# Kernel optimization log

Measured on AMD Instinct MI355X. Metric: run time of the kernel, lower is better.

## Reference

```python
import jax, jax.numpy as jnp
import numpy as np

B, L, D, H = 4, 2048, 1024, 16
DK = D // H  # 64


def setup_inputs() -> dict:
    key = jax.random.key(0)
    ks = jax.random.split(key, 5)
    x = jax.random.normal(ks[0], (B, L, D), dtype=jnp.float32)
    scale = 1.0 / np.sqrt(D)
    W_qkv = jax.random.normal(ks[1], (D, 3 * D), dtype=jnp.float32) * scale
    b_qkv = jnp.zeros((3 * D,), dtype=jnp.float32)
    W_out = jax.random.normal(ks[2], (D, D), dtype=jnp.float32) * scale
    b_out = jnp.zeros((D,), dtype=jnp.float32)
    return {"x": x, "W_qkv": W_qkv, "b_qkv": b_qkv, "W_out": W_out, "b_out": b_out}


def reference(x, W_qkv, b_qkv, W_out, b_out):
    Bx, Lx, Dx = x.shape
    qkv = x @ W_qkv + b_qkv                      # [B, L, 3D]
    q, k, v = jnp.split(qkv, 3, axis=-1)
    # [B, H, L, d_k]
    q = q.reshape(Bx, Lx, H, DK).transpose(0, 2, 1, 3)
    k = k.reshape(Bx, Lx, H, DK).transpose(0, 2, 1, 3)
    v = v.reshape(Bx, Lx, H, DK).transpose(0, 2, 1, 3)
    scores = jnp.einsum('bhqd,bhkd->bhqk', q, k) / np.sqrt(DK)
    causal = jnp.tril(jnp.ones((Lx, Lx), dtype=bool))
    scores = jnp.where(causal[None, None], scores, -jnp.inf)
    attn = jax.nn.softmax(scores, axis=-1)       # [B, H, L, L]
    out = jnp.einsum('bhqk,bhkd->bhqd', attn, v)
    out = out.transpose(0, 2, 1, 3).reshape(Bx, Lx, Dx)
    return out @ W_out + b_out
```

## Files before the change

kernel.cpp:

```cpp
#include <hip/hip_runtime.h>
#include <stdint.h>

#define B_ 4
#define L_ 2048
#define D_ 1024
#define H_ 16
#define DK_ 64

typedef __attribute__((ext_vector_type(8))) short bf16x8;
typedef __attribute__((ext_vector_type(4))) float f32x4;
typedef unsigned short bfu;

#define MFMA(a, b, c) __builtin_amdgcn_mfma_f32_16x16x32_bf16((a), (b), (c), 0, 0, 0)

__device__ __forceinline__ unsigned short f2bf(float f) {
  union { float f; unsigned int u; } v; v.f = f;
  unsigned int u = v.u;
  return (unsigned short)((u + 0x7fffu + ((u >> 16) & 1u)) >> 16);
}

__device__ __forceinline__ void gll16(const void* g, void* l) {
  __builtin_amdgcn_global_load_lds(
      (const __attribute__((address_space(1))) void*)g,
      (__attribute__((address_space(3))) void*)l, 16, 0, 0);
}

#define VMCNT(n_) asm volatile("s_waitcnt vmcnt(" #n_ ")" ::: "memory")
#define BARRIER() asm volatile("s_barrier" ::: "memory")

template <int N> __device__ __forceinline__ void vmwait() {
  static_assert(N >= 0 && N <= 8, "vmcnt range");
  if constexpr (N == 0) VMCNT(0);
  else if constexpr (N == 1) VMCNT(1);
  else if constexpr (N == 2) VMCNT(2);
  else if constexpr (N == 3) VMCNT(3);
  else if constexpr (N == 4) VMCNT(4);
  else if constexpr (N == 5) VMCNT(5);
  else if constexpr (N == 6) VMCNT(6);
  else if constexpr (N == 7) VMCNT(7);
  else VMCNT(8);
}


__global__ __launch_bounds__(256) void cast_x(const float* __restrict__ in,
                                              bfu* __restrict__ out, int n4) {
  int i = blockIdx.x * 256 + threadIdx.x;
  if (i >= n4) return;
  float4 v = ((const float4*)in)[i];
  ushort4 o;
  o.x = f2bf(v.x); o.y = f2bf(v.y); o.z = f2bf(v.z); o.w = f2bf(v.w);
  ((ushort4*)out)[i] = o;
}

__global__ void transpose_cast(const float* __restrict__ in, bfu* __restrict__ out,
                               int R, int C) {
  __shared__ float tile[32][33];
  int c0 = blockIdx.x * 32, r0 = blockIdx.y * 32;
  int tx = threadIdx.x, ty = threadIdx.y;
#pragma unroll
  for (int i = ty; i < 32; i += 8)
    tile[i][tx] = in[(size_t)(r0 + i) * C + c0 + tx];
  __syncthreads();
#pragma unroll
  for (int i = ty; i < 32; i += 8)
    out[(size_t)(c0 + i) * R + r0 + tx] = f2bf(tile[tx][i]);
}


template <int EPI, int BM, int BN, int WM, int WN>
__global__ __launch_bounds__(512, 4) void gemm8(
    const bfu* __restrict__ A, const bfu* __restrict__ Bt,
    const float* __restrict__ bias, bfu* __restrict__ Qg, bfu* __restrict__ Kg,
    bfu* __restrict__ Vtg, float* __restrict__ Out, int M, int N, int K) {
  __shared__ __align__(16) bfu LDSb[(BM + BN) * 128];
  constexpr int RM = BM / WM, RN = BN / WN;
  constexpr int MH = RM / 32, NH = RN / 32;
  constexpr int HA = BM / 128, HB = BN / 128;
  constexpr int LO = HA + HB;

  const int tid = threadIdx.x;
  const int lane = tid & 63;
  const int w = tid >> 6;
  const int wm = w / WN, wn = w % WN;
  const int l15 = lane & 15, l4 = lane >> 4;

  const int nwg = gridDim.x;
  const int cpx = nwg >> 3;
  const int bid = (int)blockIdx.x;
  const int swz = (bid & 7) * cpx + (bid >> 3);
  const int MT = M / BM;
  const int m0 = (swz % MT) * BM;
  const int n0 = (swz / MT) * BN;

  auto stageA = [&](int t, int half) {
    bfu* lb = LDSb + (t & 1) * (BM * 64);
#pragma unroll
    for (int j = 0; j < HA; ++j) {
      int idx = j * 512 + tid;
      int u = idx >> 3;
      int row = half * (RM / 2) + (u & (RM / 2 - 1)) + (u / (RM / 2)) * RM;
      int c16 = (idx & 7) ^ (row & 7);
      gll16(A + (size_t)(m0 + row) * K + t * 64 + c16 * 8,
            (char*)lb + row * 128 + (idx & 7) * 16);
    }
  };
  auto stageB = [&](int t, int half) {
    bfu* lb = LDSb + 2 * BM * 64 + (t & 1) * (BN * 64);
#pragma unroll
    for (int j = 0; j < HB; ++j) {
      int idx = j * 512 + tid;
      int u = idx >> 3;
      int row = half * (RN / 2) + (u & (RN / 2 - 1)) + (u / (RN / 2)) * RN;
      int c16 = (idx & 7) ^ (row & 7);
      gll16(Bt + (size_t)(n0 + row) * K + t * 64 + c16 * 8,
            (char*)lb + row * 128 + (idx & 7) * 16);
    }
  };

  f32x4 acc[2 * MH][2 * NH] = {};
  bf16x8 af[MH][2], bfLO[NH][2], bfHI[NH][2];

  auto lda = [&](int c, int half) {
    const char* base = (const char*)(LDSb + c * (BM * 64));
#pragma unroll
    for (int mi = 0; mi < MH; ++mi)
#pragma unroll
      for (int kk = 0; kk < 2; ++kk) {
        int row = wm * RM + half * (RM / 2) + mi * 16 + l15;
        int ch = (kk * 4 + l4) ^ (row & 7);
        af[mi][kk] = *(const bf16x8*)(base + row * 128 + ch * 16);
      }
  };
  auto ldb = [&](int c, int half, bf16x8 (&dst)[NH][2]) {
    const char* base = (const char*)(LDSb + 2 * BM * 64 + c * (BN * 64));
#pragma unroll
    for (int ni = 0; ni < NH; ++ni)
#pragma unroll
      for (int kk = 0; kk < 2; ++kk) {
        int row = wn * RN + half * (RN / 2) + ni * 16 + l15;
        int ch = (kk * 4 + l4) ^ (row & 7);
        dst[ni][kk] = *(const bf16x8*)(base + row * 128 + ch * 16);
      }
  };
  auto mm = [&](int mo, int no, bf16x8 (&bx)[NH][2]) {
    __builtin_amdgcn_s_setprio(1);
#pragma unroll
    for (int mi = 0; mi < MH; ++mi)
#pragma unroll
      for (int ni = 0; ni < NH; ++ni)
#pragma unroll
        for (int kk = 0; kk < 2; ++kk)
          acc[mo + mi][no + ni] = MFMA(af[mi][kk], bx[ni][kk], acc[mo + mi][no + ni]);
    __builtin_amdgcn_s_setprio(0);
  };

  stageA(0, 0); stageB(0, 0); stageB(0, 1); stageA(0, 1);
  vmwait<HB + HA>();
  BARRIER();

  const int NT = K >> 6;
  for (int t = 0; t < NT - 1; ++t) {
    const int c = t & 1, tn = t + 1;
    lda(c, 0); ldb(c, 0, bfLO);
    stageA(tn, 0); stageB(tn, 0);
    mm(0, 0, bfLO);
    vmwait<HA + LO>(); BARRIER();
    ldb(c, 1, bfHI);
    stageB(tn, 1);
    mm(0, NH, bfHI);
    vmwait<LO + HB>(); BARRIER();
    lda(c, 1);
    stageA(tn, 1);
    mm(MH, NH, bfHI);
    BARRIER();
    mm(MH, 0, bfLO);
    vmwait<HB + HA>(); BARRIER();
  }
  {
    const int c = (NT - 1) & 1;
    lda(c, 0); ldb(c, 0, bfLO);
    mm(0, 0, bfLO);
    vmwait<HA>(); BARRIER();
    ldb(c, 1, bfHI);
    mm(0, NH, bfHI);
    vmwait<0>(); BARRIER();
    lda(c, 1);
    mm(MH, NH, bfHI);
    mm(MH, 0, bfLO);
  }

  if constexpr (EPI == 1) {
#pragma unroll
    for (int ni = 0; ni < 2 * NH; ++ni) {
      int gn = n0 + wn * RN + ni * 16 + l15;
      float bv = bias[gn];
#pragma unroll
      for (int mi = 0; mi < 2 * MH; ++mi)
#pragma unroll
        for (int rg = 0; rg < 4; ++rg) {
          int gm = m0 + wm * RM + mi * 16 + l4 * 4 + rg;
          Out[(size_t)gm * N + gn] = acc[mi][ni][rg] + bv;
        }
    }
  } else {
    const int sec = n0 >> 10;
    if (sec < 2) {
      bfu* dst = (sec == 0) ? Qg : Kg;
      const float scale = (sec == 0) ? 0.18033688011112042f : 1.0f;
#pragma unroll
      for (int ni = 0; ni < 2 * NH; ++ni) {
        int gn = n0 + wn * RN + ni * 16 + l15;
        int rem = gn & 1023;
        int hh = rem >> 6, dk = rem & 63;
        float bv = bias[gn];
#pragma unroll
        for (int mi = 0; mi < 2 * MH; ++mi)
#pragma unroll
          for (int rg = 0; rg < 4; ++rg) {
            int gm = m0 + wm * RM + mi * 16 + l4 * 4 + rg;
            int bb = gm >> 11, ll = gm & 2047;
            dst[(((size_t)(bb * H_ + hh)) * L_ + ll) * DK_ + dk] =
                f2bf((acc[mi][ni][rg] + bv) * scale);
          }
      }
    } else {
      __syncthreads();
#pragma unroll
      for (int ni = 0; ni < 2 * NH; ++ni) {
        int n_local = wn * RN + ni * 16 + l15;
        int gn = n0 + n_local;
        float bv = bias[gn];
        int swzn = (n_local & 7) << 4;
#pragma unroll
        for (int mi = 0; mi < 2 * MH; ++mi) {
          int m_base = wm * RM + mi * 16 + l4 * 4;
          int k6 = m_base & 63;
          int p0 = (m_base & ~63) |
                   ((k6 & 32) | (((k6 >> 2) & 3) << 3) | (((k6 >> 4) & 1) << 2));
          float v0 = acc[mi][ni][0] + bv, v1 = acc[mi][ni][1] + bv;
          float v2 = acc[mi][ni][2] + bv, v3 = acc[mi][ni][3] + bv;
          uint32_t w01, w23;
          asm("v_cvt_pk_bf16_f32 %0, %1, %2" : "=v"(w01) : "v"(v0), "v"(v1));
          asm("v_cvt_pk_bf16_f32 %0, %1, %2" : "=v"(w23) : "v"(v2), "v"(v3));
          *(uint32_t*)((char*)LDSb + n_local * (BM * 2) + ((2 * p0) ^ swzn)) = w01;
          *(uint32_t*)((char*)LDSb + n_local * (BM * 2) + ((2 * p0 + 4) ^ swzn)) = w23;
        }
      }
      __syncthreads();
      int n = tid >> 2;
      int cb = (tid & 3) * 4;
      int gnn = n0 + n;
      int hh = (gnn >> 6) & 15, dk = gnn & 63;
      size_t rowbase =
          (((size_t)((m0 >> 11) * H_ + hh)) * DK_ + dk) * L_ + (m0 & 2047);
#pragma unroll
      for (int j = 0; j < 4; ++j) {
        int ch = cb + j;
        bf16x8 vv = *(const bf16x8*)((char*)LDSb + n * (BM * 2) +
                                     ((ch * 16) ^ ((n & 7) << 4)));
        *(bf16x8*)(Vtg + rowbase + ch * 8) = vv;
      }
    }
  }
}


__global__ __launch_bounds__(256, 3) void attn(const bfu* __restrict__ Qg,
                                               const bfu* __restrict__ Kg,
                                               const bfu* __restrict__ Vtg,
                                               bfu* __restrict__ Ao) {
  __shared__ __align__(16) bfu Ks[2 * 64 * 64];
  __shared__ __align__(16) bfu Vs[2 * 64 * 64];

  const int tid = threadIdx.x;
  const int lane = tid & 63;
  const int w = tid >> 6;
  const int l15 = lane & 15, l4 = lane >> 4;

  const int hid = blockIdx.x;
  const int xcd = hid & 7, slot = hid >> 3;
  const int bh = xcd * 8 + (slot >> 3);
  const int p = slot & 7;
  const int b = bh >> 4, h = bh & 15;

  for (int seg = 0; seg < 2; ++seg) {
    const int qb = (seg == 0) ? p : 15 - p;
    const int q0 = qb * 128;
    const int nt = 2 * qb + 2;
    const int q0w = q0 + w * 32;

    bf16x8 qf[2][2];
#pragma unroll
    for (int mi = 0; mi < 2; ++mi)
#pragma unroll
      for (int kk = 0; kk < 2; ++kk)
        qf[mi][kk] = *(const bf16x8*)(
            Qg + ((size_t)bh * L_ + q0w + mi * 16 + l15) * DK_ + kk * 32 + l4 * 8);

#pragma unroll
    for (int i = 0; i < 2; ++i) {
      int lb = i * 256 + tid;
      int r = lb >> 3, c16 = (lb & 7) ^ (r & 7);
      gll16(Kg + ((size_t)bh * L_ + r) * DK_ + c16 * 8, (char*)Ks + lb * 16);
      gll16(Vtg + ((size_t)bh * DK_ + r) * L_ + c16 * 8, (char*)Vs + lb * 16);
    }
    VMCNT(0);
    BARRIER();

    f32x4 acco[2][4] = {};
    float m[2] = {-1e30f, -1e30f};
    float l[2] = {0.f, 0.f};

    for (int t = 0; t < nt; ++t) {
      const int cur = t & 1;
      const int kv0 = t * 64;
      const char* Kc = (const char*)Ks + cur * 8192;
      const char* Vc = (const char*)Vs + cur * 8192;

      if (t + 1 < nt) {
        const int nb = (t + 1) & 1, nkv = (t + 1) * 64;
#pragma unroll
        for (int i = 0; i < 2; ++i) {
          int lb = i * 256 + tid;
          int r = lb >> 3, c16 = (lb & 7) ^ (r & 7);
          gll16(Kg + ((size_t)bh * L_ + nkv + r) * DK_ + c16 * 8,
                (char*)Ks + nb * 8192 + lb * 16);
          gll16(Vtg + ((size_t)bh * DK_ + r) * L_ + nkv + c16 * 8,
                (char*)Vs + nb * 8192 + lb * 16);
        }
        VMCNT(4);
      } else {
        VMCNT(0);
      }
      BARRIER();

      if (kv0 <= q0w + 31) {
        f32x4 s[2][4] = {};
        __builtin_amdgcn_s_setprio(1);
#pragma unroll
        for (int kk = 0; kk < 2; ++kk)
#pragma unroll
          for (int ni = 0; ni < 4; ++ni) {
            int r = ni * 16 + l15;
            int ch = (kk * 4 + l4) ^ (r & 7);
            bf16x8 kf = *(const bf16x8*)(Kc + r * 128 + ch * 16);
#pragma unroll
            for (int mi = 0; mi < 2; ++mi)
              s[mi][ni] = MFMA(kf, qf[mi][kk], s[mi][ni]);
          }
        __builtin_amdgcn_s_setprio(0);

        if (kv0 + 63 > q0w) {
#pragma unroll
          for (int mi = 0; mi < 2; ++mi) {
            int qg_ = q0w + mi * 16 + l15;
#pragma unroll
            for (int ni = 0; ni < 4; ++ni) {
              int kvg = kv0 + ni * 16 + l4 * 4;
#pragma unroll
              for (int rg = 0; rg < 4; ++rg)
                if (kvg + rg > qg_) s[mi][ni][rg] = -1e30f;
            }
          }
        }

        float mx[2];
#pragma unroll
        for (int mi = 0; mi < 2; ++mi) {
          float v = fmaxf(fmaxf(fmaxf(s[mi][0][0], s[mi][0][1]),
                                fmaxf(s[mi][0][2], s[mi][0][3])),
                          fmaxf(fmaxf(s[mi][1][0], s[mi][1][1]),
                                fmaxf(s[mi][1][2], s[mi][1][3])));
          v = fmaxf(v, fmaxf(fmaxf(fmaxf(s[mi][2][0], s[mi][2][1]),
                                   fmaxf(s[mi][2][2], s[mi][2][3])),
                             fmaxf(fmaxf(s[mi][3][0], s[mi][3][1]),
                                   fmaxf(s[mi][3][2], s[mi][3][3]))));
          v = fmaxf(v, __shfl_xor(v, 16));
          v = fmaxf(v, __shfl_xor(v, 32));
          mx[mi] = v;
        }
        float grow = fmaxf(mx[0] - m[0], mx[1] - m[1]);
        if (__any(grow > 11.0f)) {
#pragma unroll
          for (int mi = 0; mi < 2; ++mi) {
            float mn = fmaxf(m[mi], mx[mi]);
            float sc = __builtin_amdgcn_exp2f(m[mi] - mn);
            m[mi] = mn;
            l[mi] *= sc;
#pragma unroll
            for (int rg = 0; rg < 4; ++rg) {
              float scq = __shfl(sc, l4 * 4 + rg);
              acco[mi][0][rg] *= scq; acco[mi][1][rg] *= scq;
              acco[mi][2][rg] *= scq; acco[mi][3][rg] *= scq;
            }
          }
        }

        uint32_t pk[2][4][2];
#pragma unroll
        for (int mi = 0; mi < 2; ++mi)
#pragma unroll
          for (int ni = 0; ni < 4; ++ni) {
            float p0 = __builtin_amdgcn_exp2f(s[mi][ni][0] - m[mi]);
            float p1 = __builtin_amdgcn_exp2f(s[mi][ni][1] - m[mi]);
            float p2 = __builtin_amdgcn_exp2f(s[mi][ni][2] - m[mi]);
            float p3 = __builtin_amdgcn_exp2f(s[mi][ni][3] - m[mi]);
            l[mi] += (p0 + p1) + (p2 + p3);
            asm("v_cvt_pk_bf16_f32 %0, %1, %2" : "=v"(pk[mi][ni][0]) : "v"(p0), "v"(p1));
            asm("v_cvt_pk_bf16_f32 %0, %1, %2" : "=v"(pk[mi][ni][1]) : "v"(p2), "v"(p3));
          }

        __builtin_amdgcn_s_setprio(1);
#pragma unroll
        for (int kk = 0; kk < 2; ++kk) {
          union { uint32_t wd[4]; bf16x8 v; } u[2];
#pragma unroll
          for (int mi = 0; mi < 2; ++mi) {
            u[mi].wd[0] = pk[mi][2 * kk][0];
            u[mi].wd[1] = pk[mi][2 * kk][1];
            u[mi].wd[2] = pk[mi][2 * kk + 1][0];
            u[mi].wd[3] = pk[mi][2 * kk + 1][1];
          }
#pragma unroll
          for (int ni = 0; ni < 4; ++ni) {
            int r = ni * 16 + l15;
            int ch = (kk * 4 + l4) ^ (r & 7);
            bf16x8 vf = *(const bf16x8*)(Vc + r * 128 + ch * 16);
#pragma unroll
            for (int mi = 0; mi < 2; ++mi)
              acco[mi][ni] = MFMA(u[mi].v, vf, acco[mi][ni]);
          }
        }
        __builtin_amdgcn_s_setprio(0);
      }

      BARRIER();
    }

#pragma unroll
    for (int mi = 0; mi < 2; ++mi) {
      float ls = l[mi];
      ls += __shfl_xor(ls, 16);
      ls += __shfl_xor(ls, 32);
      float linv = 1.0f / ls;
#pragma unroll
      for (int rg = 0; rg < 4; ++rg) {
        float lq = __shfl(linv, l4 * 4 + rg);
        int q = q0w + mi * 16 + l4 * 4 + rg;
#pragma unroll
        for (int ni = 0; ni < 4; ++ni) {
          int d = ni * 16 + l15;
          Ao[((size_t)b * L_ + q) * D_ + h * DK_ + d] = f2bf(acco[mi][ni][rg] * lq);
        }
      }
    }
  }
}


extern "C" void kernel_launch(void* const* d_in, const int* in_sizes, int n_in,
                              void* d_out, int out_size, void* d_ws, size_t ws_size,
                              hipStream_t stream) {
  const float* x = (const float*)d_in[0];
  const float* W_qkv = (const float*)d_in[1];
  const float* b_qkv = (const float*)d_in[2];
  const float* W_out = (const float*)d_in[3];
  const float* b_out = (const float*)d_in[4];
  float* out = (float*)d_out;

  char* ws = (char*)d_ws;
  bfu* xb     = (bfu*)(ws);
  bfu* Wqkv_t = (bfu*)(ws + 16777216);
  bfu* Wout_t = (bfu*)(ws + 23068672);
  bfu* Qg     = (bfu*)(ws + 25165824);
  bfu* Kg     = (bfu*)(ws + 41943040);
  bfu* Vtg    = (bfu*)(ws + 58720256);
  bfu* Ao     = (bfu*)(ws + 75497472);

  cast_x<<<8192, 256, 0, stream>>>(x, xb, 2097152);
  transpose_cast<<<dim3(96, 32), dim3(32, 8), 0, stream>>>(W_qkv, Wqkv_t, 1024, 3072);
  transpose_cast<<<dim3(32, 32), dim3(32, 8), 0, stream>>>(W_out, Wout_t, 1024, 1024);

  gemm8<0, 128, 128, 4, 2><<<1536, 512, 0, stream>>>(xb, Wqkv_t, b_qkv, Qg, Kg,
                                                     Vtg, nullptr, 8192, 3072, 1024);
  attn<<<512, 256, 0, stream>>>(Qg, Kg, Vtg, Ao);
  gemm8<1, 128, 128, 4, 2><<<512, 512, 0, stream>>>(Ao, Wout_t, b_out, nullptr,
                                                    nullptr, nullptr, out, 8192,
                                                    1024, 1024);
}
```

Baseline: 181.8 us.

## Replace double-buffered 8-wave GEMM with single-buffered 64x64-per-wave GEMM

Rewrites the projection GEMM as a simpler single-buffered kernel in which each wave owns a 64x64 tile. The QKV projection now uses 128x256 block tiles across 8 waves, and the output projection uses 128x128 tiles across 4 waves. Block swizzling is changed to walk N within groups of 8 M-tiles, and the V-transpose epilogue now runs in 128-column passes. This removes the half-tile interleaved prefetch pipeline, so global loads are no longer overlapped with MFMA inside a block, which risks stalls on the two barriers per K step. In exchange it gets larger per-wave reuse and halved LDS use, which allows more resident blocks.

```diff
diff --git a/kernel.cpp b/kernel.cpp
--- a/kernel.cpp
+++ b/kernel.cpp
@@ -27,19 +27,6 @@
 
 #define VMCNT(n_) asm volatile("s_waitcnt vmcnt(" #n_ ")" ::: "memory")
 #define BARRIER() asm volatile("s_barrier" ::: "memory")
-
-template <int N> __device__ __forceinline__ void vmwait() {
-  static_assert(N >= 0 && N <= 8, "vmcnt range");
-  if constexpr (N == 0) VMCNT(0);
-  else if constexpr (N == 1) VMCNT(1);
-  else if constexpr (N == 2) VMCNT(2);
-  else if constexpr (N == 3) VMCNT(3);
-  else if constexpr (N == 4) VMCNT(4);
-  else if constexpr (N == 5) VMCNT(5);
-  else if constexpr (N == 6) VMCNT(6);
-  else if constexpr (N == 7) VMCNT(7);
-  else VMCNT(8);
-}
 
 
 __global__ __launch_bounds__(256) void cast_x(const float* __restrict__ in,
@@ -67,16 +54,15 @@
 }
 
 
-template <int EPI, int BM, int BN, int WM, int WN>
-__global__ __launch_bounds__(512, 4) void gemm8(
+template <int EPI, int BM, int BN, int WM, int WN, int OCC>
+__global__ __launch_bounds__(WM * WN * 64, OCC) void gemm_s(
     const bfu* __restrict__ A, const bfu* __restrict__ Bt,
     const float* __restrict__ bias, bfu* __restrict__ Qg, bfu* __restrict__ Kg,
     bfu* __restrict__ Vtg, float* __restrict__ Out, int M, int N, int K) {
-  __shared__ __align__(16) bfu LDSb[(BM + BN) * 128];
+  __shared__ __align__(16) bfu LDSb[(BM + BN) * 64];
+  constexpr int TH = WM * WN * 64;
   constexpr int RM = BM / WM, RN = BN / WN;
-  constexpr int MH = RM / 32, NH = RN / 32;
-  constexpr int HA = BM / 128, HB = BN / 128;
-  constexpr int LO = HA + HB;
+  static_assert(RM == 64 && RN == 64, "per-wave tile is 64x64");
 
   const int tid = threadIdx.x;
   const int lane = tid & 63;
@@ -88,114 +74,88 @@
   const int cpx = nwg >> 3;
   const int bid = (int)blockIdx.x;
   const int swz = (bid & 7) * cpx + (bid >> 3);
-  const int MT = M / BM;
-  const int m0 = (swz % MT) * BM;
-  const int n0 = (swz / MT) * BN;
-
-  auto stageA = [&](int t, int half) {
-    bfu* lb = LDSb + (t & 1) * (BM * 64);
-#pragma unroll
-    for (int j = 0; j < HA; ++j) {
-      int idx = j * 512 + tid;
-      int u = idx >> 3;
-      int row = half * (RM / 2) + (u & (RM / 2 - 1)) + (u / (RM / 2)) * RM;
-      int c16 = (idx & 7) ^ (row & 7);
+  const int NTt = N / BN;
+  const int m0 = ((swz & 7) + 8 * (swz / (8 * NTt))) * BM;
+  const int n0 = ((swz >> 3) % NTt) * BN;
+
+  auto stageA = [&](int t) {
+    char* lb = (char*)LDSb;
+#pragma unroll
+    for (int j = 0; j < BM * 8 / TH; ++j) {
+      int idx = j * TH + tid;
+      int row = idx >> 3, c16p = idx & 7;
+      int c16 = c16p ^ (row & 7);
       gll16(A + (size_t)(m0 + row) * K + t * 64 + c16 * 8,
-            (char*)lb + row * 128 + (idx & 7) * 16);
+            lb + row * 128 + c16p * 16);
     }
   };
-  auto stageB = [&](int t, int half) {
-    bfu* lb = LDSb + 2 * BM * 64 + (t & 1) * (BN * 64);
-#pragma unroll
-    for (int j = 0; j < HB; ++j) {
-      int idx = j * 512 + tid;
-      int u = idx >> 3;
-      int row = half * (RN / 2) + (u & (RN / 2 - 1)) + (u / (RN / 2)) * RN;
-      int c16 = (idx & 7) ^ (row & 7);
+  auto stageB = [&](int t) {
+    char* lb = (char*)(LDSb + BM * 64);
+#pragma unroll
+    for (int j = 0; j < BN * 8 / TH; ++j) {
+      int idx = j * TH + tid;
+      int row = idx >> 3, c16p = idx & 7;
+      int c16 = c16p ^ (row & 7);
       gll16(Bt + (size_t)(n0 + row) * K + t * 64 + c16 * 8,
-            (char*)lb + row * 128 + (idx & 7) * 16);
+            lb + row * 128 + c16p * 16);
     }
   };
 
-  f32x4 acc[2 * MH][2 * NH] = {};
-  bf16x8 af[MH][2], bfLO[NH][2], bfHI[NH][2];
-
-  auto lda = [&](int c, int half) {
-    const char* base = (const char*)(LDSb + c * (BM * 64));
-#pragma unroll
-    for (int mi = 0; mi < MH; ++mi)
+  f32x4 acc[4][4] = {};
+  bf16x8 af[4][2], bfh[2][2];
+
+  auto lda = [&]() {
+    const char* base = (const char*)LDSb;
+#pragma unroll
+    for (int mi = 0; mi < 4; ++mi)
 #pragma unroll
       for (int kk = 0; kk < 2; ++kk) {
-        int row = wm * RM + half * (RM / 2) + mi * 16 + l15;
+        int row = wm * RM + mi * 16 + l15;
         int ch = (kk * 4 + l4) ^ (row & 7);
         af[mi][kk] = *(const bf16x8*)(base + row * 128 + ch * 16);
       }
   };
-  auto ldb = [&](int c, int half, bf16x8 (&dst)[NH][2]) {
-    const char* base = (const char*)(LDSb + 2 * BM * 64 + c * (BN * 64));
-#pragma unroll
-    for (int ni = 0; ni < NH; ++ni)
+  auto ldb = [&](int half) {
+    const char* base = (const char*)(LDSb + BM * 64);
+#pragma unroll
+    for (int ni = 0; ni < 2; ++ni)
 #pragma unroll
       for (int kk = 0; kk < 2; ++kk) {
-        int row = wn * RN + half * (RN / 2) + ni * 16 + l15;
+        int row = wn * RN + half * 32 + ni * 16 + l15;
         int ch = (kk * 4 + l4) ^ (row & 7);
-        dst[ni][kk] = *(const bf16x8*)(base + row * 128 + ch * 16);
+        bfh[ni][kk] = *(const bf16x8*)(base + row * 128 + ch * 16);
       }
   };
-  auto mm = [&](int mo, int no, bf16x8 (&bx)[NH][2]) {
+  auto mmh = [&](int half) {
     __builtin_amdgcn_s_setprio(1);
 #pragma unroll
-    for (int mi = 0; mi < MH; ++mi)
-#pragma unroll
-      for (int ni = 0; ni < NH; ++ni)
+    for (int mi = 0; mi < 4; ++mi)
+#pragma unroll
+      for (int ni = 0; ni < 2; ++ni)
 #pragma unroll
         for (int kk = 0; kk < 2; ++kk)
-          acc[mo + mi][no + ni] = MFMA(af[mi][kk], bx[ni][kk], acc[mo + mi][no + ni]);
+          acc[mi][half * 2 + ni] =
+              MFMA(af[mi][kk], bfh[ni][kk], acc[mi][half * 2 + ni]);
     __builtin_amdgcn_s_setprio(0);
   };
 
-  stageA(0, 0); stageB(0, 0); stageB(0, 1); stageA(0, 1);
-  vmwait<HB + HA>();
-  BARRIER();
-
   const int NT = K >> 6;
-  for (int t = 0; t < NT - 1; ++t) {
-    const int c = t & 1, tn = t + 1;
-    lda(c, 0); ldb(c, 0, bfLO);
-    stageA(tn, 0); stageB(tn, 0);
-    mm(0, 0, bfLO);
-    vmwait<HA + LO>(); BARRIER();
-    ldb(c, 1, bfHI);
-    stageB(tn, 1);
-    mm(0, NH, bfHI);
-    vmwait<LO + HB>(); BARRIER();
-    lda(c, 1);
-    stageA(tn, 1);
-    mm(MH, NH, bfHI);
-    BARRIER();
-    mm(MH, 0, bfLO);
-    vmwait<HB + HA>(); BARRIER();
+  for (int t = 0; t < NT; ++t) {
+    __syncthreads();
+    stageA(t); stageB(t);
+    __syncthreads();
+    lda();
+    ldb(0); mmh(0);
+    ldb(1); mmh(1);
   }
-  {
-    const int c = (NT - 1) & 1;
-    lda(c, 0); ldb(c, 0, bfLO);
-    mm(0, 0, bfLO);
-    vmwait<HA>(); BARRIER();
-    ldb(c, 1, bfHI);
-    mm(0, NH, bfHI);
-    vmwait<0>(); BARRIER();
-    lda(c, 1);
-    mm(MH, NH, bfHI);
-    mm(MH, 0, bfLO);
-  }
 
   if constexpr (EPI == 1) {
 #pragma unroll
-    for (int ni = 0; ni < 2 * NH; ++ni) {
+    for (int ni = 0; ni < 4; ++ni) {
       int gn = n0 + wn * RN + ni * 16 + l15;
       float bv = bias[gn];
 #pragma unroll
-      for (int mi = 0; mi < 2 * MH; ++mi)
+      for (int mi = 0; mi < 4; ++mi)
 #pragma unroll
         for (int rg = 0; rg < 4; ++rg) {
           int gm = m0 + wm * RM + mi * 16 + l4 * 4 + rg;
@@ -208,13 +168,13 @@
       bfu* dst = (sec == 0) ? Qg : Kg;
       const float scale = (sec == 0) ? 0.18033688011112042f : 1.0f;
 #pragma unroll
-      for (int ni = 0; ni < 2 * NH; ++ni) {
+      for (int ni = 0; ni < 4; ++ni) {
         int gn = n0 + wn * RN + ni * 16 + l15;
         int rem = gn & 1023;
         int hh = rem >> 6, dk = rem & 63;
         float bv = bias[gn];
 #pragma unroll
-        for (int mi = 0; mi < 2 * MH; ++mi)
+        for (int mi = 0; mi < 4; ++mi)
 #pragma unroll
           for (int rg = 0; rg < 4; ++rg) {
             int gm = m0 + wm * RM + mi * 16 + l4 * 4 + rg;
@@ -226,39 +186,50 @@
     } else {
       __syncthreads();
 #pragma unroll
-      for (int ni = 0; ni < 2 * NH; ++ni) {
-        int n_local = wn * RN + ni * 16 + l15;
-        int gn = n0 + n_local;
-        float bv = bias[gn];
-        int swzn = (n_local & 7) << 4;
-#pragma unroll
-        for (int mi = 0; mi < 2 * MH; ++mi) {
-          int m_base = wm * RM + mi * 16 + l4 * 4;
-          int k6 = m_base & 63;
-          int p0 = (m_base & ~63) |
-                   ((k6 & 32) | (((k6 >> 2) & 3) << 3) | (((k6 >> 4) & 1) << 2));
-          float v0 = acc[mi][ni][0] + bv, v1 = acc[mi][ni][1] + bv;
-          float v2 = acc[mi][ni][2] + bv, v3 = acc[mi][ni][3] + bv;
-          uint32_t w01, w23;
-          asm("v_cvt_pk_bf16_f32 %0, %1, %2" : "=v"(w01) : "v"(v0), "v"(v1));
-          asm("v_cvt_pk_bf16_f32 %0, %1, %2" : "=v"(w23) : "v"(v2), "v"(v3));
-          *(uint32_t*)((char*)LDSb + n_local * (BM * 2) + ((2 * p0) ^ swzn)) = w01;
-          *(uint32_t*)((char*)LDSb + n_local * (BM * 2) + ((2 * p0 + 4) ^ swzn)) = w23;
-        }
-      }
-      __syncthreads();
-      int n = tid >> 2;
-      int cb = (tid & 3) * 4;
-      int gnn = n0 + n;
-      int hh = (gnn >> 6) & 15, dk = gnn & 63;
-      size_t rowbase =
-          (((size_t)((m0 >> 11) * H_ + hh)) * DK_ + dk) * L_ + (m0 & 2047);
-#pragma unroll
-      for (int j = 0; j < 4; ++j) {
-        int ch = cb + j;
-        bf16x8 vv = *(const bf16x8*)((char*)LDSb + n * (BM * 2) +
-                                     ((ch * 16) ^ ((n & 7) << 4)));
-        *(bf16x8*)(Vtg + rowbase + ch * 8) = vv;
+      for (int pass = 0; pass < BN / 128; ++pass) {
+        if (wn * RN >= pass * 128 && wn * RN < pass * 128 + 128) {
+#pragma unroll
+          for (int ni = 0; ni < 4; ++ni) {
+            int n_local = wn * RN + ni * 16 + l15;
+            int n_rel = n_local - pass * 128;
+            int gn = n0 + n_local;
+            float bv = bias[gn];
+            int swzn = (n_rel & 7) << 4;
+#pragma unroll
+            for (int mi = 0; mi < 4; ++mi) {
+              int m_base = wm * RM + mi * 16 + l4 * 4;
+              int k6 = m_base & 63;
+              int p0 = (m_base & ~63) |
+                       ((k6 & 32) | (((k6 >> 2) & 3) << 3) | (((k6 >> 4) & 1) << 2));
+              float v0 = acc[mi][ni][0] + bv, v1 = acc[mi][ni][1] + bv;
+              float v2 = acc[mi][ni][2] + bv, v3 = acc[mi][ni][3] + bv;
+              uint32_t w01, w23;
+              asm("v_cvt_pk_bf16_f32 %0, %1, %2" : "=v"(w01) : "v"(v0), "v"(v1));
+              asm("v_cvt_pk_bf16_f32 %0, %1, %2" : "=v"(w23) : "v"(v2), "v"(v3));
+              *(uint32_t*)((char*)LDSb + n_rel * (BM * 2) + ((2 * p0) ^ swzn)) = w01;
+              *(uint32_t*)((char*)LDSb + n_rel * (BM * 2) + ((2 * p0 + 4) ^ swzn)) = w23;
+            }
+          }
+        }
+        __syncthreads();
+        if (TH >= 512 || true) {
+          int n = tid >> 2;
+          if (n < 128) {
+            int cb = (tid & 3) * 4;
+            int gnn = n0 + pass * 128 + n;
+            int hh = (gnn >> 6) & 15, dk = gnn & 63;
+            size_t rowbase =
+                (((size_t)((m0 >> 11) * H_ + hh)) * DK_ + dk) * L_ + (m0 & 2047);
+#pragma unroll
+            for (int j = 0; j < 4; ++j) {
+              int ch = cb + j;
+              bf16x8 vv = *(const bf16x8*)((char*)LDSb + n * (BM * 2) +
+                                           ((ch * 16) ^ ((n & 7) << 4)));
+              *(bf16x8*)(Vtg + rowbase + ch * 8) = vv;
+            }
+          }
+        }
+        __syncthreads();
       }
     }
   }
@@ -481,10 +452,9 @@
   transpose_cast<<<dim3(96, 32), dim3(32, 8), 0, stream>>>(W_qkv, Wqkv_t, 1024, 3072);
   transpose_cast<<<dim3(32, 32), dim3(32, 8), 0, stream>>>(W_out, Wout_t, 1024, 1024);
 
-  gemm8<0, 128, 128, 4, 2><<<1536, 512, 0, stream>>>(xb, Wqkv_t, b_qkv, Qg, Kg,
-                                                     Vtg, nullptr, 8192, 3072, 1024);
+  gemm_s<0, 128, 256, 2, 4, 4><<<768, 512, 0, stream>>>(
+      xb, Wqkv_t, b_qkv, Qg, Kg, Vtg, nullptr, 8192, 3072, 1024);
   attn<<<512, 256, 0, stream>>>(Qg, Kg, Vtg, Ao);
-  gemm8<1, 128, 128, 4, 2><<<512, 512, 0, stream>>>(Ao, Wout_t, b_out, nullptr,
-                                                    nullptr, nullptr, out, 8192,
-                                                    1024, 1024);
-}
+  gemm_s<1, 128, 128, 2, 2, 3><<<512, 256, 0, stream>>>(
+      Ao, Wout_t, b_out, nullptr, nullptr, nullptr, out, 8192, 1024, 1024);
+}
```

New measurement: 181.7 us. About the same (-0.0%).
